# Performance work log

Measured on AMD Instinct MI355X. Metric: run time of the kernel, lower is better.

Reference implementation:

```python
import jax, jax.numpy as jnp
import numpy as np

N_NODES = 170000
N_EDGES = 1200000
IN_FEATS = 128
N_HIDDEN = 256
N_CLASSES = 40
BN_EPS = 1e-5


def setup_inputs() -> dict:
    key = jax.random.key(0)
    ks = jax.random.split(key, 12)
    feat = jax.random.normal(ks[0], (N_NODES, IN_FEATS), dtype=jnp.float32)
    src = jax.random.randint(ks[1], (N_EDGES,), 0, N_NODES, dtype=jnp.int32)
    dst = jax.random.randint(ks[2], (N_EDGES,), 0, N_NODES, dtype=jnp.int32)
    # GraphConv weights (glorot-ish scale) and last-layer bias
    W0 = jax.random.normal(ks[3], (IN_FEATS, N_HIDDEN), dtype=jnp.float32) * (1.0 / np.sqrt(IN_FEATS))
    W1 = jax.random.normal(ks[4], (N_HIDDEN, N_HIDDEN), dtype=jnp.float32) * (1.0 / np.sqrt(N_HIDDEN))
    W2 = jax.random.normal(ks[5], (N_HIDDEN, N_CLASSES), dtype=jnp.float32) * (1.0 / np.sqrt(N_HIDDEN))
    b2 = jnp.zeros((N_CLASSES,), dtype=jnp.float32)
    # BatchNorm affine params for the two hidden layers
    g0 = jnp.ones((N_HIDDEN,), dtype=jnp.float32)
    beta0 = jnp.zeros((N_HIDDEN,), dtype=jnp.float32)
    g1 = jnp.ones((N_HIDDEN,), dtype=jnp.float32)
    beta1 = jnp.zeros((N_HIDDEN,), dtype=jnp.float32)
    return {"feat": feat, "src": src, "dst": dst, "W0": W0, "W1": W1, "W2": W2,
            "b2": b2, "g0": g0, "beta0": beta0, "g1": g1, "beta1": beta1}


def _batchnorm(h, gamma, beta):
    mean = jnp.mean(h, axis=0)
    var = jnp.mean((h - mean) ** 2, axis=0)  # biased var, torch training-mode norm
    return (h - mean) * jax.lax.rsqrt(var + BN_EPS) * gamma + beta


def reference(feat, src, dst, W0, W1, W2, b2, g0, beta0, g1, beta1):
    n = feat.shape[0]
    ones_e = jnp.ones(src.shape, dtype=feat.dtype)
    deg_out = jnp.clip(jax.ops.segment_sum(ones_e, src, num_segments=n), 1.0)
    deg_in = jnp.clip(jax.ops.segment_sum(ones_e, dst, num_segments=n), 1.0)
    norm_src = deg_out ** -0.5  # [N]
    norm_dst = deg_in ** -0.5   # [N]

    def conv(h, W, bias=None):
        # GraphConv 'both': D_out^{-1/2} message, sum-aggregate, D_in^{-1/2}
        h = h @ W                              # project first (out <= in)
        msg = h[src] * norm_src[src][:, None]  # [E, out]
        agg = jax.ops.segment_sum(msg, dst, num_segments=n) * norm_dst[:, None]
        if bias is not None:
            agg = agg + bias
        return agg

    # dropout layers are identity in this deterministic (eval-style) reference
    h = conv(feat, W0)
    h = jax.nn.relu(_batchnorm(h, g0, beta0))
    h = conv(h, W1)
    h = jax.nn.relu(_batchnorm(h, g1, beta1))
    h = conv(h, W2, b2)
    return h
```

## Files before the change

### kernel.cpp

```cpp
#include <hip/hip_runtime.h>

#define NN 170000
#define NE 1200000
#define F_IN 128
#define F_HID 256
#define F_OUT 40
#define BN_EPS 1e-5f
#define SCAN_B ((NN + 255) / 256)
#define GB_TILES ((NN + 127) / 128)
#define STAT_ROWS (2 * GB_TILES)
#define STAT_CHUNK 32
#define STAT_NCH ((STAT_ROWS + STAT_CHUNK - 1) / STAT_CHUNK)

typedef __attribute__((ext_vector_type(8))) short short8;
typedef __attribute__((ext_vector_type(4))) float f32x4;
typedef __attribute__((ext_vector_type(4))) unsigned short us4;
typedef __attribute__((ext_vector_type(4))) unsigned int u32x4;

__device__ __forceinline__ float b2f(unsigned short u) {
    union { unsigned x; float f; } c; c.x = ((unsigned)u) << 16; return c.f;
}
__device__ __forceinline__ unsigned short f2b(float f) {
    union { float f; unsigned x; } c; c.f = f;
    unsigned r = (c.x + 0x7FFFu + ((c.x >> 16) & 1u)) >> 16;
    return (unsigned short)r;
}
__device__ __forceinline__ unsigned bn2(unsigned u, float a0, float b0, float a1, float b1) {
    float lo = b2f((unsigned short)(u & 0xffffu));
    float hi = b2f((unsigned short)(u >> 16));
    lo = fmaxf(lo * a0 + b0, 0.0f);
    hi = fmaxf(hi * a1 + b1, 0.0f);
    return (unsigned)f2b(lo) | ((unsigned)f2b(hi) << 16);
}

__global__ void count_kernel(const int* __restrict__ src, const int* __restrict__ dst,
                             int* __restrict__ cnt_src, int* __restrict__ cnt_dst, int E) {
    int e = blockIdx.x * blockDim.x + threadIdx.x;
    if (e < E) {
        atomicAdd(&cnt_src[src[e]], 1);
        atomicAdd(&cnt_dst[dst[e]], 1);
    }
}

__global__ void norm_kernel(const int* __restrict__ cnt_src, const int* __restrict__ cnt_dst,
                            float* __restrict__ norm_src, float* __restrict__ norm_dst, int N) {
    int i = blockIdx.x * blockDim.x + threadIdx.x;
    if (i < N) {
        norm_src[i] = rsqrtf((float)max(cnt_src[i], 1));
        norm_dst[i] = rsqrtf((float)max(cnt_dst[i], 1));
    }
}

__global__ void scan_block_kernel(const int* __restrict__ cnt, int* __restrict__ local,
                                  int* __restrict__ partials, int N) {
    __shared__ int s[256];
    int t = threadIdx.x;
    int idx = blockIdx.x * 256 + t;
    int v = (idx < N) ? cnt[idx] : 0;
    s[t] = v;
    __syncthreads();
    #pragma unroll
    for (int off = 1; off < 256; off <<= 1) {
        int x = (t >= off) ? s[t - off] : 0;
        __syncthreads();
        s[t] += x;
        __syncthreads();
    }
    if (idx < N) local[idx] = s[t] - v;
    if (t == 255) partials[blockIdx.x] = s[t];
}

__global__ void scan_partials_kernel(int* __restrict__ partials, int B) {
    __shared__ int s[1024];
    int t = threadIdx.x;
    int v = (t < B) ? partials[t] : 0;
    s[t] = v;
    __syncthreads();
    #pragma unroll
    for (int off = 1; off < 1024; off <<= 1) {
        int x = (t >= off) ? s[t - off] : 0;
        __syncthreads();
        s[t] += x;
        __syncthreads();
    }
    if (t < B) partials[t] = s[t] - v;
}

__global__ void scan_add_kernel(const int* __restrict__ local, const int* __restrict__ partials,
                                int* __restrict__ row_ptr, int N) {
    int idx = blockIdx.x * blockDim.x + threadIdx.x;
    if (idx < N) row_ptr[idx] = local[idx] + partials[idx >> 8];
    if (idx == 0) row_ptr[N] = NE;
}

__global__ void fill_kernel(const int* __restrict__ src, const int* __restrict__ dst,
                            const int* __restrict__ row_ptr, int* __restrict__ fill,
                            int* __restrict__ csr_src, int E) {
    int e = blockIdx.x * blockDim.x + threadIdx.x;
    if (e < E) {
        int d = dst[e];
        int pos = row_ptr[d] + atomicAdd(&fill[d], 1);
        csr_src[pos] = src[e];
    }
}

__global__ void cast_feat_kernel(const float* __restrict__ feat, const float* __restrict__ norm_src,
                                 unsigned short* __restrict__ featb) {
    unsigned idx = blockIdx.x * blockDim.x + threadIdx.x;
    if (idx >= (unsigned)NN * (F_IN / 4)) return;
    float ns = norm_src[idx / (F_IN / 4)];
    f32x4 v = __builtin_nontemporal_load((const f32x4*)(feat + (size_t)idx * 4));
    us4 o; o.x = f2b(v.x * ns); o.y = f2b(v.y * ns); o.z = f2b(v.z * ns); o.w = f2b(v.w * ns);
    *(us4*)(featb + (size_t)idx * 4) = o;
}

__global__ void apply_bn_scale_kernel(const unsigned short* __restrict__ in,
                                      const float* __restrict__ bna, const float* __restrict__ bnb,
                                      const float* __restrict__ norm_src,
                                      unsigned short* __restrict__ outp) {
    unsigned idx = blockIdx.x * blockDim.x + threadIdx.x;
    if (idx >= (unsigned)NN * (F_HID / 8)) return;
    unsigned row = idx / (F_HID / 8);
    unsigned c8 = (idx % (F_HID / 8)) * 8;
    float ns = norm_src[row];
    u32x4 u = *(const u32x4*)(in + (size_t)idx * 8);
    const f32x4 a0 = *(const f32x4*)(bna + c8);
    const f32x4 a1 = *(const f32x4*)(bna + c8 + 4);
    const f32x4 s0 = *(const f32x4*)(bnb + c8);
    const f32x4 s1 = *(const f32x4*)(bnb + c8 + 4);
    u.x = bn2(u.x, a0.x * ns, s0.x * ns, a0.y * ns, s0.y * ns);
    u.y = bn2(u.y, a0.z * ns, s0.z * ns, a0.w * ns, s0.w * ns);
    u.z = bn2(u.z, a1.x * ns, s1.x * ns, a1.y * ns, s1.y * ns);
    u.w = bn2(u.w, a1.z * ns, s1.z * ns, a1.w * ns, s1.w * ns);
    __builtin_nontemporal_store(u, (u32x4*)(outp + (size_t)idx * 8));
}

template<int F>
__global__ void gather_sum_kernel(const unsigned short* __restrict__ h, const int* __restrict__ row_ptr,
                                  const int* __restrict__ csr_src,
                                  unsigned short* __restrict__ out, int N) {
    constexpr int TPN = F / 4;
    unsigned idx = blockIdx.x * blockDim.x + threadIdx.x;
    if (idx >= (unsigned)N * TPN) return;
    unsigned node = idx / TPN;
    unsigned g = idx % TPN;
    int beg = row_ptr[node], end = row_ptr[node + 1];
    float ax0 = 0.f, ay0 = 0.f, az0 = 0.f, aw0 = 0.f;
    float ax1 = 0.f, ay1 = 0.f, az1 = 0.f, aw1 = 0.f;
    int e = beg;
    for (; e + 2 <= end; e += 2) {
        int s0 = csr_src[e], s1 = csr_src[e + 1];
        const us4 v0 = *(const us4*)(h + (size_t)s0 * F + g * 4);
        const us4 v1 = *(const us4*)(h + (size_t)s1 * F + g * 4);
        ax0 += b2f(v0.x); ay0 += b2f(v0.y); az0 += b2f(v0.z); aw0 += b2f(v0.w);
        ax1 += b2f(v1.x); ay1 += b2f(v1.y); az1 += b2f(v1.z); aw1 += b2f(v1.w);
    }
    if (e < end) {
        int s0 = csr_src[e];
        const us4 v0 = *(const us4*)(h + (size_t)s0 * F + g * 4);
        ax0 += b2f(v0.x); ay0 += b2f(v0.y); az0 += b2f(v0.z); aw0 += b2f(v0.w);
    }
    us4 o;
    o.x = f2b(ax0 + ax1); o.y = f2b(ay0 + ay1); o.z = f2b(az0 + az1); o.w = f2b(aw0 + aw1);
    __builtin_nontemporal_store(o, (us4*)(out + (size_t)node * F + g * 4));
}

__global__ void gather_final_kernel(const float* __restrict__ h, const int* __restrict__ row_ptr,
                                    const int* __restrict__ csr_src,
                                    const float* __restrict__ norm_dst, const float* __restrict__ bias,
                                    float* __restrict__ out, int N) {
    constexpr int TPN = F_OUT / 4;
    unsigned idx = blockIdx.x * blockDim.x + threadIdx.x;
    if (idx >= (unsigned)N * TPN) return;
    unsigned node = idx / TPN;
    unsigned g = idx % TPN;
    int beg = row_ptr[node], end = row_ptr[node + 1];
    float ax0 = 0.f, ay0 = 0.f, az0 = 0.f, aw0 = 0.f;
    float ax1 = 0.f, ay1 = 0.f, az1 = 0.f, aw1 = 0.f;
    int e = beg;
    for (; e + 2 <= end; e += 2) {
        int s0 = csr_src[e], s1 = csr_src[e + 1];
        const f32x4 v0 = *(const f32x4*)(h + (size_t)s0 * F_OUT + g * 4);
        const f32x4 v1 = *(const f32x4*)(h + (size_t)s1 * F_OUT + g * 4);
        ax0 += v0.x; ay0 += v0.y; az0 += v0.z; aw0 += v0.w;
        ax1 += v1.x; ay1 += v1.y; az1 += v1.z; aw1 += v1.w;
    }
    if (e < end) {
        int s0 = csr_src[e];
        const f32x4 v0 = *(const f32x4*)(h + (size_t)s0 * F_OUT + g * 4);
        ax0 += v0.x; ay0 += v0.y; az0 += v0.z; aw0 += v0.w;
    }
    float nd = norm_dst[node];
    const f32x4 b = *(const f32x4*)(bias + g * 4);
    f32x4 r;
    r.x = (ax0 + ax1) * nd + b.x; r.y = (ay0 + ay1) * nd + b.y;
    r.z = (az0 + az1) * nd + b.z; r.w = (aw0 + aw1) * nd + b.w;
    __builtin_nontemporal_store(r, (f32x4*)(out + (size_t)node * F_OUT + g * 4));
}

template<int K, int M, int MP>
__global__ void wt_kernel(const float* __restrict__ W, unsigned short* __restrict__ Wt) {
    int idx = blockIdx.x * blockDim.x + threadIdx.x;
    if (idx >= MP * K) return;
    int m = idx / K, k = idx % K;
    float v = (m < M) ? W[(size_t)k * M + m] : 0.0f;
    Wt[idx] = f2b(v);
}

__global__ void stat_reduce_kernel(const float* __restrict__ part, float* __restrict__ red) {
    int c = threadIdx.x;
    int ch = blockIdx.x;
    int r0 = ch * STAT_CHUNK;
    int r1 = min(r0 + STAT_CHUNK, STAT_ROWS);
    float s = 0.f;
    for (int r = r0; r < r1; r++) s += part[(size_t)r * 512 + c];
    red[ch * 512 + c] = s;
}

__global__ void bn_finalize2_kernel(const float* __restrict__ red,
                                    const float* __restrict__ gamma, const float* __restrict__ beta,
                                    float* __restrict__ a, float* __restrict__ b) {
    int c = threadIdx.x;
    float sum = 0.f, sumsq = 0.f;
    for (int ch = 0; ch < STAT_NCH; ch++) {
        sum   += red[ch * 512 + c];
        sumsq += red[ch * 512 + 256 + c];
    }
    float invN = 1.0f / (float)NN;
    float mean = sum * invN;
    float var = sumsq * invN - mean * mean;
    float inv = rsqrtf(var + BN_EPS);
    float ac = inv * gamma[c];
    a[c] = ac;
    b[c] = beta[c] - mean * ac;
}

template<int K, int BN_T, int WM_T, int WN_T, int WAVES_N, bool SCALE, bool BF16OUT, int M_OUT,
         bool STATS, bool APPLYBN>
__global__ __launch_bounds__(256) void mfma_gemm(const unsigned short* __restrict__ A,
                                                 const unsigned short* __restrict__ Wt,
                                                 const float* __restrict__ rowscale,
                                                 void* __restrict__ C,
                                                 const float* __restrict__ bna,
                                                 const float* __restrict__ bnb,
                                                 float* __restrict__ opart, int N) {
    constexpr int BM = 128, BK = 64, AP = 72;
    constexpr int WAVES_M = 4 / WAVES_N;
    __shared__ unsigned short As[BM * AP];
    __shared__ unsigned short Bs[BN_T * AP];

    const int lane = threadIdx.x & 63;
    const int wave = threadIdx.x >> 6;
    const int wr = wave / WAVES_N, wc = wave % WAVES_N;
    const int quad = lane >> 4, l15 = lane & 15;
    const int r0 = blockIdx.y * BM;
    const int c0 = blockIdx.x * BN_T;
    const int wmb = wr * WM_T * 16;
    const int wnb = wc * WN_T * 16;

    f32x4 acc[WM_T][WN_T] = {};

    for (int k0 = 0; k0 < K; k0 += BK) {
        #pragma unroll
        for (int p = 0; p < BM * (BK / 8) / 256; p++) {
            int c = threadIdx.x + p * 256;
            int row = c >> 3, off = (c & 7) * 8;
            int gr = r0 + row;
            u32x4 v = {0u, 0u, 0u, 0u};
            if (gr < N) {
                v = *(const u32x4*)(A + (size_t)gr * K + k0 + off);
                if (APPLYBN) {
                    int kb = k0 + off;
                    const f32x4 a0 = *(const f32x4*)(bna + kb);
                    const f32x4 a1 = *(const f32x4*)(bna + kb + 4);
                    const f32x4 s0 = *(const f32x4*)(bnb + kb);
                    const f32x4 s1 = *(const f32x4*)(bnb + kb + 4);
                    v.x = bn2(v.x, a0.x, s0.x, a0.y, s0.y);
                    v.y = bn2(v.y, a0.z, s0.z, a0.w, s0.w);
                    v.z = bn2(v.z, a1.x, s1.x, a1.y, s1.y);
                    v.w = bn2(v.w, a1.z, s1.z, a1.w, s1.w);
                }
            }
            *(u32x4*)(As + row * AP + off) = v;
        }
        #pragma unroll
        for (int p = 0; p < BN_T * (BK / 8) / 256; p++) {
            int c = threadIdx.x + p * 256;
            int m = c >> 3, off = (c & 7) * 8;
            *(u32x4*)(Bs + m * AP + off) = *(const u32x4*)(Wt + (size_t)(c0 + m) * K + k0 + off);
        }
        __syncthreads();
        #pragma unroll
        for (int kk = 0; kk < BK; kk += 32) {
            short8 af[WM_T], bf[WN_T];
            #pragma unroll
            for (int i = 0; i < WM_T; i++)
                af[i] = *(const short8*)(As + (wmb + i * 16 + l15) * AP + kk + quad * 8);
            #pragma unroll
            for (int j = 0; j < WN_T; j++)
                bf[j] = *(const short8*)(Bs + (wnb + j * 16 + l15) * AP + kk + quad * 8);
            #pragma unroll
            for (int i = 0; i < WM_T; i++)
                #pragma unroll
                for (int j = 0; j < WN_T; j++)
                    acc[i][j] = __builtin_amdgcn_mfma_f32_16x16x32_bf16(af[i], bf[j], acc[i][j], 0, 0, 0);
        }
        __syncthreads();
    }

    float s[WN_T] = {}, ss[WN_T] = {};
    #pragma unroll
    for (int i = 0; i < WM_T; i++) {
        #pragma unroll
        for (int r = 0; r < 4; r++) {
            int row = r0 + wmb + i * 16 + quad * 4 + r;
            if (row >= N) continue;
            float scale = SCALE ? rowscale[row] : 1.0f;
            #pragma unroll
            for (int j = 0; j < WN_T; j++) {
                float v = acc[i][j][r] * scale;
                if (STATS) { s[j] += v; ss[j] += v * v; }
                int col = c0 + wnb + j * 16 + l15;
                if (col < M_OUT) {
                    if (BF16OUT) ((unsigned short*)C)[(size_t)row * M_OUT + col] = f2b(v);
                    else         ((float*)C)[(size_t)row * M_OUT + col] = v;
                }
            }
        }
    }
    if (STATS) {
        #pragma unroll
        for (int j = 0; j < WN_T; j++) {
            float t = s[j], t2 = ss[j];
            t  += __shfl_xor(t, 16);  t  += __shfl_xor(t, 32);
            t2 += __shfl_xor(t2, 16); t2 += __shfl_xor(t2, 32);
            if (quad == 0) {
                int col = c0 + wnb + j * 16 + l15;
                size_t prow = (size_t)(blockIdx.y * WAVES_M + wr) * 512;
                opart[prow + col] = t;
                opart[prow + 256 + col] = t2;
            }
        }
    }
}

extern "C" void kernel_launch(void* const* d_in, const int* in_sizes, int n_in,
                              void* d_out, int out_size, void* d_ws, size_t ws_size,
                              hipStream_t stream) {
    const float* feat  = (const float*)d_in[0];
    const int*   src   = (const int*)d_in[1];
    const int*   dst   = (const int*)d_in[2];
    const float* W0    = (const float*)d_in[3];
    const float* W1    = (const float*)d_in[4];
    const float* W2    = (const float*)d_in[5];
    const float* b2    = (const float*)d_in[6];
    const float* g0    = (const float*)d_in[7];
    const float* beta0 = (const float*)d_in[8];
    const float* g1    = (const float*)d_in[9];
    const float* beta1 = (const float*)d_in[10];
    float* out = (float*)d_out;

    const int N = NN, E = NE;

    char* ws = (char*)d_ws;
    auto alloc_b = [&](size_t bytes) {
        void* p = (void*)ws;
        ws += ((bytes + 255) / 256) * 256;
        return p;
    };
    float* norm_src = (float*)alloc_b((size_t)N * 4);
    float* norm_dst = (float*)alloc_b((size_t)N * 4);
    int*   row_ptr  = (int*)alloc_b((size_t)(N + 1) * 4);
    int*   csr_src  = (int*)alloc_b((size_t)E * 4);
    float* bnpart   = (float*)alloc_b((size_t)STAT_ROWS * 512 * 4);
    float* bnred    = (float*)alloc_b((size_t)STAT_NCH * 512 * 4);
    float* bn_a0    = (float*)alloc_b(256 * 4);
    float* bn_b0    = (float*)alloc_b(256 * 4);
    float* bn_a1    = (float*)alloc_b(256 * 4);
    float* bn_b1    = (float*)alloc_b(256 * 4);
    unsigned short* Wt0 = (unsigned short*)alloc_b((size_t)256 * 128 * 2);
    unsigned short* Wt1 = (unsigned short*)alloc_b((size_t)256 * 256 * 2);
    unsigned short* Wt2 = (unsigned short*)alloc_b((size_t)64 * 256 * 2);
    void* B1 = alloc_b((size_t)N * 512);
    void* B2 = alloc_b((size_t)N * 512);
    unsigned short* featb = (unsigned short*)alloc_b((size_t)N * F_IN * 2);

    unsigned short* B1b = (unsigned short*)B1;
    unsigned short* B2b = (unsigned short*)B2;
    float*          B2f = (float*)B2;

    int* cnt_src  = (int*)B1;
    int* cnt_dst  = cnt_src + N;
    int* fill     = cnt_dst + N;
    int* local    = fill + N;
    int* partials = local + N;

    hipMemsetAsync(cnt_src, 0, ((size_t)4 * N + 1024) * 4, stream);
    count_kernel<<<(E + 255) / 256, 256, 0, stream>>>(src, dst, cnt_src, cnt_dst, E);
    norm_kernel<<<(N + 255) / 256, 256, 0, stream>>>(cnt_src, cnt_dst, norm_src, norm_dst, N);
    scan_block_kernel<<<SCAN_B, 256, 0, stream>>>(cnt_dst, local, partials, N);
    scan_partials_kernel<<<1, 1024, 0, stream>>>(partials, SCAN_B);
    scan_add_kernel<<<(N + 255) / 256, 256, 0, stream>>>(local, partials, row_ptr, N);
    fill_kernel<<<(E + 255) / 256, 256, 0, stream>>>(src, dst, row_ptr, fill, csr_src, E);
    wt_kernel<128, 256, 256><<<(256 * 128 + 255) / 256, 256, 0, stream>>>(W0, Wt0);
    wt_kernel<256, 256, 256><<<(256 * 256 + 255) / 256, 256, 0, stream>>>(W1, Wt1);
    wt_kernel<256, 40, 64><<<(64 * 256 + 255) / 256, 256, 0, stream>>>(W2, Wt2);
    cast_feat_kernel<<<((unsigned)N * (F_IN / 4) + 255) / 256, 256, 0, stream>>>(feat, norm_src, featb);

    const int GB = GB_TILES;

    {
        unsigned total = (unsigned)N * (F_IN / 4);
        gather_sum_kernel<F_IN><<<(total + 255) / 256, 256, 0, stream>>>(featb, row_ptr, csr_src, B1b, N);
    }
    mfma_gemm<128, 128, 4, 4, 2, true, true, 256, true, false><<<dim3(2, GB), 256, 0, stream>>>(
        B1b, Wt0, norm_dst, B2, nullptr, nullptr, bnpart, N);
    stat_reduce_kernel<<<STAT_NCH, 512, 0, stream>>>(bnpart, bnred);
    bn_finalize2_kernel<<<1, 256, 0, stream>>>(bnred, g0, beta0, bn_a0, bn_b0);

    apply_bn_scale_kernel<<<((unsigned)N * (F_HID / 8) + 255) / 256, 256, 0, stream>>>(
        B2b, bn_a0, bn_b0, norm_src, B1b);
    {
        unsigned total = (unsigned)N * (F_HID / 4);
        gather_sum_kernel<F_HID><<<(total + 255) / 256, 256, 0, stream>>>(B1b, row_ptr, csr_src, B2b, N);
    }
    mfma_gemm<256, 128, 4, 4, 2, true, true, 256, true, false><<<dim3(2, GB), 256, 0, stream>>>(
        B2b, Wt1, norm_dst, B1, nullptr, nullptr, bnpart, N);
    stat_reduce_kernel<<<STAT_NCH, 512, 0, stream>>>(bnpart, bnred);
    bn_finalize2_kernel<<<1, 256, 0, stream>>>(bnred, g1, beta1, bn_a1, bn_b1);

    mfma_gemm<256, 64, 2, 4, 1, true, false, 40, false, true><<<dim3(1, GB), 256, 0, stream>>>(
        B1b, Wt2, norm_src, B2, bn_a1, bn_b1, nullptr, N);
    {
        unsigned total = (unsigned)N * (F_OUT / 4);
        gather_final_kernel<<<(total + 255) / 256, 256, 0, stream>>>(
            B2f, row_ptr, csr_src, norm_dst, b2, out, N);
    }
}
```

Before: 830.9 us.

## Fuse BN+ReLU+norm into gather and drop LDS staging in MFMA GEMM

Removes the separate apply_bn_scale pass by applying BatchNorm affine, ReLU and the source-degree scale inside the layer-2 gather, so each neighbour's features are transformed on the fly. This saves a full read and write of the hidden activation, but repeats the BN math and adds a norm_src load for every edge. The GEMM also stops staging A and W tiles in shared memory and instead loads MFMA fragments straight from global memory, adding a launch-bounds occupancy hint. That drops the __syncthreads barriers and LDS traffic but relies on cache hits for the reuse that shared memory used to provide. Buffers are reassigned to match the new data flow.

```diff
diff --git a/kernel.cpp b/kernel.cpp
--- a/kernel.cpp
+++ b/kernel.cpp
@@ -114,36 +114,22 @@
     *(us4*)(featb + (size_t)idx * 4) = o;
 }
 
-__global__ void apply_bn_scale_kernel(const unsigned short* __restrict__ in,
-                                      const float* __restrict__ bna, const float* __restrict__ bnb,
-                                      const float* __restrict__ norm_src,
-                                      unsigned short* __restrict__ outp) {
-    unsigned idx = blockIdx.x * blockDim.x + threadIdx.x;
-    if (idx >= (unsigned)NN * (F_HID / 8)) return;
-    unsigned row = idx / (F_HID / 8);
-    unsigned c8 = (idx % (F_HID / 8)) * 8;
-    float ns = norm_src[row];
-    u32x4 u = *(const u32x4*)(in + (size_t)idx * 8);
-    const f32x4 a0 = *(const f32x4*)(bna + c8);
-    const f32x4 a1 = *(const f32x4*)(bna + c8 + 4);
-    const f32x4 s0 = *(const f32x4*)(bnb + c8);
-    const f32x4 s1 = *(const f32x4*)(bnb + c8 + 4);
-    u.x = bn2(u.x, a0.x * ns, s0.x * ns, a0.y * ns, s0.y * ns);
-    u.y = bn2(u.y, a0.z * ns, s0.z * ns, a0.w * ns, s0.w * ns);
-    u.z = bn2(u.z, a1.x * ns, s1.x * ns, a1.y * ns, s1.y * ns);
-    u.w = bn2(u.w, a1.z * ns, s1.z * ns, a1.w * ns, s1.w * ns);
-    __builtin_nontemporal_store(u, (u32x4*)(outp + (size_t)idx * 8));
-}
-
-template<int F>
+template<int F, bool FUSE>
 __global__ void gather_sum_kernel(const unsigned short* __restrict__ h, const int* __restrict__ row_ptr,
                                   const int* __restrict__ csr_src,
+                                  const float* __restrict__ bna, const float* __restrict__ bnb,
+                                  const float* __restrict__ norm_src,
                                   unsigned short* __restrict__ out, int N) {
     constexpr int TPN = F / 4;
     unsigned idx = blockIdx.x * blockDim.x + threadIdx.x;
     if (idx >= (unsigned)N * TPN) return;
     unsigned node = idx / TPN;
     unsigned g = idx % TPN;
+    f32x4 ca = {0.f, 0.f, 0.f, 0.f}, cb = {0.f, 0.f, 0.f, 0.f};
+    if (FUSE) {
+        ca = *(const f32x4*)(bna + g * 4);
+        cb = *(const f32x4*)(bnb + g * 4);
+    }
     int beg = row_ptr[node], end = row_ptr[node + 1];
     float ax0 = 0.f, ay0 = 0.f, az0 = 0.f, aw0 = 0.f;
     float ax1 = 0.f, ay1 = 0.f, az1 = 0.f, aw1 = 0.f;
@@ -152,13 +138,33 @@
         int s0 = csr_src[e], s1 = csr_src[e + 1];
         const us4 v0 = *(const us4*)(h + (size_t)s0 * F + g * 4);
         const us4 v1 = *(const us4*)(h + (size_t)s1 * F + g * 4);
-        ax0 += b2f(v0.x); ay0 += b2f(v0.y); az0 += b2f(v0.z); aw0 += b2f(v0.w);
-        ax1 += b2f(v1.x); ay1 += b2f(v1.y); az1 += b2f(v1.z); aw1 += b2f(v1.w);
+        if (FUSE) {
+            float n0 = norm_src[s0], n1 = norm_src[s1];
+            ax0 += fmaxf(fmaf(b2f(v0.x), ca.x, cb.x), 0.f) * n0;
+            ay0 += fmaxf(fmaf(b2f(v0.y), ca.y, cb.y), 0.f) * n0;
+            az0 += fmaxf(fmaf(b2f(v0.z), ca.z, cb.z), 0.f) * n0;
+            aw0 += fmaxf(fmaf(b2f(v0.w), ca.w, cb.w), 0.f) * n0;
+            ax1 += fmaxf(fmaf(b2f(v1.x), ca.x, cb.x), 0.f) * n1;
+            ay1 += fmaxf(fmaf(b2f(v1.y), ca.y, cb.y), 0.f) * n1;
+            az1 += fmaxf(fmaf(b2f(v1.z), ca.z, cb.z), 0.f) * n1;
+            aw1 += fmaxf(fmaf(b2f(v1.w), ca.w, cb.w), 0.f) * n1;
+        } else {
+            ax0 += b2f(v0.x); ay0 += b2f(v0.y); az0 += b2f(v0.z); aw0 += b2f(v0.w);
+            ax1 += b2f(v1.x); ay1 += b2f(v1.y); az1 += b2f(v1.z); aw1 += b2f(v1.w);
+        }
     }
     if (e < end) {
         int s0 = csr_src[e];
         const us4 v0 = *(const us4*)(h + (size_t)s0 * F + g * 4);
-        ax0 += b2f(v0.x); ay0 += b2f(v0.y); az0 += b2f(v0.z); aw0 += b2f(v0.w);
+        if (FUSE) {
+            float n0 = norm_src[s0];
+            ax0 += fmaxf(fmaf(b2f(v0.x), ca.x, cb.x), 0.f) * n0;
+            ay0 += fmaxf(fmaf(b2f(v0.y), ca.y, cb.y), 0.f) * n0;
+            az0 += fmaxf(fmaf(b2f(v0.z), ca.z, cb.z), 0.f) * n0;
+            aw0 += fmaxf(fmaf(b2f(v0.w), ca.w, cb.w), 0.f) * n0;
+        } else {
+            ax0 += b2f(v0.x); ay0 += b2f(v0.y); az0 += b2f(v0.z); aw0 += b2f(v0.w);
+        }
     }
     us4 o;
     o.x = f2b(ax0 + ax1); o.y = f2b(ay0 + ay1); o.z = f2b(az0 + az1); o.w = f2b(aw0 + aw1);
@@ -237,18 +243,15 @@
 
 template<int K, int BN_T, int WM_T, int WN_T, int WAVES_N, bool SCALE, bool BF16OUT, int M_OUT,
          bool STATS, bool APPLYBN>
-__global__ __launch_bounds__(256) void mfma_gemm(const unsigned short* __restrict__ A,
-                                                 const unsigned short* __restrict__ Wt,
-                                                 const float* __restrict__ rowscale,
-                                                 void* __restrict__ C,
-                                                 const float* __restrict__ bna,
-                                                 const float* __restrict__ bnb,
-                                                 float* __restrict__ opart, int N) {
-    constexpr int BM = 128, BK = 64, AP = 72;
+__global__ __launch_bounds__(256, 3) void mfma_gemm(const unsigned short* __restrict__ A,
+                                                    const unsigned short* __restrict__ Wt,
+                                                    const float* __restrict__ rowscale,
+                                                    void* __restrict__ C,
+                                                    const float* __restrict__ bna,
+                                                    const float* __restrict__ bnb,
+                                                    float* __restrict__ opart, int N) {
+    constexpr int BM = 128;
     constexpr int WAVES_M = 4 / WAVES_N;
-    __shared__ unsigned short As[BM * AP];
-    __shared__ unsigned short Bs[BN_T * AP];
-
     const int lane = threadIdx.x & 63;
     const int wave = threadIdx.x >> 6;
     const int wr = wave / WAVES_N, wc = wave % WAVES_N;
@@ -258,54 +261,52 @@
     const int wmb = wr * WM_T * 16;
     const int wnb = wc * WN_T * 16;
 
+    const unsigned short* aptr[WM_T];
+    #pragma unroll
+    for (int i = 0; i < WM_T; i++) {
+        int gr = r0 + wmb + i * 16 + l15;
+        if (gr > N - 1) gr = N - 1;
+        aptr[i] = A + (size_t)gr * K + quad * 8;
+    }
+    const unsigned short* bptr[WN_T];
+    #pragma unroll
+    for (int j = 0; j < WN_T; j++)
+        bptr[j] = Wt + (size_t)(c0 + wnb + j * 16 + l15) * K + quad * 8;
+
     f32x4 acc[WM_T][WN_T] = {};
 
-    for (int k0 = 0; k0 < K; k0 += BK) {
+    #pragma unroll
+    for (int kk = 0; kk < K; kk += 32) {
+        short8 af[WM_T], bf[WN_T];
+        f32x4 a0 = {0,0,0,0}, a1 = {0,0,0,0}, s0 = {0,0,0,0}, s1 = {0,0,0,0};
+        if (APPLYBN) {
+            int kb = kk + quad * 8;
+            a0 = *(const f32x4*)(bna + kb);
+            a1 = *(const f32x4*)(bna + kb + 4);
+            s0 = *(const f32x4*)(bnb + kb);
+            s1 = *(const f32x4*)(bnb + kb + 4);
+        }
         #pragma unroll
-        for (int p = 0; p < BM * (BK / 8) / 256; p++) {
-            int c = threadIdx.x + p * 256;
-            int row = c >> 3, off = (c & 7) * 8;
-            int gr = r0 + row;
-            u32x4 v = {0u, 0u, 0u, 0u};
-            if (gr < N) {
-                v = *(const u32x4*)(A + (size_t)gr * K + k0 + off);
-                if (APPLYBN) {
-                    int kb = k0 + off;
-                    const f32x4 a0 = *(const f32x4*)(bna + kb);
-                    const f32x4 a1 = *(const f32x4*)(bna + kb + 4);
-                    const f32x4 s0 = *(const f32x4*)(bnb + kb);
-                    const f32x4 s1 = *(const f32x4*)(bnb + kb + 4);
-                    v.x = bn2(v.x, a0.x, s0.x, a0.y, s0.y);
-                    v.y = bn2(v.y, a0.z, s0.z, a0.w, s0.w);
-                    v.z = bn2(v.z, a1.x, s1.x, a1.y, s1.y);
-                    v.w = bn2(v.w, a1.z, s1.z, a1.w, s1.w);
-                }
+        for (int i = 0; i < WM_T; i++) {
+            if (APPLYBN) {
+                u32x4 u = *(const u32x4*)(aptr[i] + kk);
+                u.x = bn2(u.x, a0.x, s0.x, a0.y, s0.y);
+                u.y = bn2(u.y, a0.z, s0.z, a0.w, s0.w);
+                u.z = bn2(u.z, a1.x, s1.x, a1.y, s1.y);
+                u.w = bn2(u.w, a1.z, s1.z, a1.w, s1.w);
+                af[i] = *(short8*)&u;
+            } else {
+                af[i] = *(const short8*)(aptr[i] + kk);
             }
-            *(u32x4*)(As + row * AP + off) = v;
         }
         #pragma unroll
-        for (int p = 0; p < BN_T * (BK / 8) / 256; p++) {
-            int c = threadIdx.x + p * 256;
-            int m = c >> 3, off = (c & 7) * 8;
-            *(u32x4*)(Bs + m * AP + off) = *(const u32x4*)(Wt + (size_t)(c0 + m) * K + k0 + off);
-        }
-        __syncthreads();
+        for (int j = 0; j < WN_T; j++)
+            bf[j] = *(const short8*)(bptr[j] + kk);
         #pragma unroll
-        for (int kk = 0; kk < BK; kk += 32) {
-            short8 af[WM_T], bf[WN_T];
-            #pragma unroll
-            for (int i = 0; i < WM_T; i++)
-                af[i] = *(const short8*)(As + (wmb + i * 16 + l15) * AP + kk + quad * 8);
+        for (int i = 0; i < WM_T; i++)
             #pragma unroll
             for (int j = 0; j < WN_T; j++)
-                bf[j] = *(const short8*)(Bs + (wnb + j * 16 + l15) * AP + kk + quad * 8);
-            #pragma unroll
-            for (int i = 0; i < WM_T; i++)
-                #pragma unroll
-                for (int j = 0; j < WN_T; j++)
-                    acc[i][j] = __builtin_amdgcn_mfma_f32_16x16x32_bf16(af[i], bf[j], acc[i][j], 0, 0, 0);
-        }
-        __syncthreads();
+                acc[i][j] = __builtin_amdgcn_mfma_f32_16x16x32_bf16(af[i], bf[j], acc[i][j], 0, 0, 0);
     }
 
     float s[WN_T] = {}, ss[WN_T] = {};
@@ -387,7 +388,7 @@
 
     unsigned short* B1b = (unsigned short*)B1;
     unsigned short* B2b = (unsigned short*)B2;
-    float*          B2f = (float*)B2;
+    float*          B1f = (float*)B1;
 
     int* cnt_src  = (int*)B1;
     int* cnt_dst  = cnt_src + N;
@@ -411,29 +412,29 @@
 
     {
         unsigned total = (unsigned)N * (F_IN / 4);
-        gather_sum_kernel<F_IN><<<(total + 255) / 256, 256, 0, stream>>>(featb, row_ptr, csr_src, B1b, N);
+        gather_sum_kernel<F_IN, false><<<(total + 255) / 256, 256, 0, stream>>>(
+            featb, row_ptr, csr_src, nullptr, nullptr, nullptr, B1b, N);
     }
     mfma_gemm<128, 128, 4, 4, 2, true, true, 256, true, false><<<dim3(2, GB), 256, 0, stream>>>(
         B1b, Wt0, norm_dst, B2, nullptr, nullptr, bnpart, N);
     stat_reduce_kernel<<<STAT_NCH, 512, 0, stream>>>(bnpart, bnred);
     bn_finalize2_kernel<<<1, 256, 0, stream>>>(bnred, g0, beta0, bn_a0, bn_b0);
 
-    apply_bn_scale_kernel<<<((unsigned)N * (F_HID / 8) + 255) / 256, 256, 0, stream>>>(
-        B2b, bn_a0, bn_b0, norm_src, B1b);
     {
         unsigned total = (unsigned)N * (F_HID / 4);
-        gather_sum_kernel<F_HID><<<(total + 255) / 256, 256, 0, stream>>>(B1b, row_ptr, csr_src, B2b, N);
+        gather_sum_kernel<F_HID, true><<<(total + 255) / 256, 256, 0, stream>>>(
+            B2b, row_ptr, csr_src, bn_a0, bn_b0, norm_src, B1b, N);
     }
     mfma_gemm<256, 128, 4, 4, 2, true, true, 256, true, false><<<dim3(2, GB), 256, 0, stream>>>(
-        B2b, Wt1, norm_dst, B1, nullptr, nullptr, bnpart, N);
+        B1b, Wt1, norm_dst, B2, nullptr, nullptr, bnpart, N);
     stat_reduce_kernel<<<STAT_NCH, 512, 0, stream>>>(bnpart, bnred);
     bn_finalize2_kernel<<<1, 256, 0, stream>>>(bnred, g1, beta1, bn_a1, bn_b1);
 
     mfma_gemm<256, 64, 2, 4, 1, true, false, 40, false, true><<<dim3(1, GB), 256, 0, stream>>>(
-        B1b, Wt2, norm_src, B2, bn_a1, bn_b1, nullptr, N);
+        B2b, Wt2, norm_src, B1, bn_a1, bn_b1, nullptr, N);
     {
         unsigned total = (unsigned)N * (F_OUT / 4);
         gather_final_kernel<<<(total + 255) / 256, 256, 0, stream>>>(
-            B2f, row_ptr, csr_src, norm_dst, b2, out, N);
-    }
-}
+            B1f, row_ptr, csr_src, norm_dst, b2, out, N);
+    }
+}
```

Result: faster. 799.8 us (-3.7%).
